# Performance work log

Measured on AMD Instinct MI355X. Metric: run time of the kernel, lower is better.

## Reference

```python
import jax, jax.numpy as jnp
import numpy as np

N_NODES = 50000
N_EDGES = 800000
NUM_GRAPHS = 64
D_IN = 128
D_HID = 128
D_EMB = 128
D_PRED = 256
D_OUT = 1
BN_EPS = 1e-5


def gcn_conv(x, W, b, src, dst, n_nodes):
    # PyG GCNConv: add self-loops, sym-normalize, aggregate, then bias.
    h = x @ W  # [N, d_out]
    # in-degree with self-loops
    deg = jax.ops.segment_sum(jnp.ones((src.shape[0],), h.dtype), dst,
                              num_segments=n_nodes) + 1.0
    inv_sqrt = 1.0 / jnp.sqrt(deg)  # [N]
    norm = inv_sqrt[src] * inv_sqrt[dst]  # [E]
    msg = h[src] * norm[:, None]  # [E, d_out] gather + scale
    agg = jax.ops.segment_sum(msg, dst, num_segments=n_nodes)
    # self-loop contribution: norm_ii = 1/deg_i
    agg = agg + h / deg[:, None]
    return agg + b


def batch_norm(h, gamma, beta):
    # BatchNorm1d in training mode: batch stats, biased variance
    mean = jnp.mean(h, axis=0)
    var = jnp.mean(jnp.square(h - mean), axis=0)
    return (h - mean) / jnp.sqrt(var + BN_EPS) * gamma + beta


def setup_inputs() -> dict:
    key = jax.random.key(0)
    ks = jax.random.split(key, 12)
    x = jax.random.normal(ks[0], (N_NODES, D_IN), dtype=jnp.float32)
    edge_index = jax.random.randint(ks[1], (2, N_EDGES), 0, N_NODES, dtype=jnp.int32)
    batch = jnp.sort(jax.random.randint(ks[2], (N_NODES,), 0, NUM_GRAPHS, dtype=jnp.int32))
    s1 = 1.0 / np.sqrt(D_IN)
    s2 = 1.0 / np.sqrt(D_HID)
    s3 = 1.0 / np.sqrt(D_EMB)
    s4 = 1.0 / np.sqrt(D_PRED)
    return {
        "x": x,
        "edge_index": edge_index,
        "batch": batch,
        "W1": jax.random.uniform(ks[3], (D_IN, D_HID), jnp.float32, -s1, s1),
        "b1": jnp.zeros((D_HID,), jnp.float32),
        "g1": jnp.ones((D_HID,), jnp.float32),
        "be1": jnp.zeros((D_HID,), jnp.float32),
        "W2": jax.random.uniform(ks[4], (D_HID, D_EMB), jnp.float32, -s2, s2),
        "b2": jnp.zeros((D_EMB,), jnp.float32),
        "g2": jnp.ones((D_EMB,), jnp.float32),
        "be2": jnp.zeros((D_EMB,), jnp.float32),
        "Wp1": jax.random.uniform(ks[5], (D_EMB, D_PRED), jnp.float32, -s3, s3),
        "bp1": jax.random.uniform(ks[6], (D_PRED,), jnp.float32, -s3, s3),
        "Wp2": jax.random.uniform(ks[7], (D_PRED, D_OUT), jnp.float32, -s4, s4),
        "bp2": jax.random.uniform(ks[8], (D_OUT,), jnp.float32, -s4, s4),
    }


def reference(x, edge_index, batch, W1, b1, g1, be1, W2, b2, g2, be2, Wp1, bp1, Wp2, bp2):
    src, dst = edge_index[0], edge_index[1]
    h = gcn_conv(x, W1, b1, src, dst, N_NODES)
    h = batch_norm(jax.nn.relu(h), g1, be1)
    h = gcn_conv(h, W2, b2, src, dst, N_NODES)
    h = batch_norm(jax.nn.relu(h), g2, be2)
    # global max pool per graph
    pooled = jax.ops.segment_max(h, batch, num_segments=NUM_GRAPHS)  # [G, D_EMB]
    # predictor MLP (Dropout is identity in eval)
    z = jax.nn.relu(pooled @ Wp1 + bp1)
    return z @ Wp2 + bp2
```

## Files before the change

### kernel.cpp

```cpp
#include <hip/hip_runtime.h>

#define NN 50000
#define NE 800000
#define NG 64
#define D 128
#define DP 256
#define BN_EPS 1e-5f
#define NSLOT 32
#define NB 196
#define NEB 3125

typedef unsigned short bf16;
typedef __attribute__((ext_vector_type(8))) short s16x8;
typedef __attribute__((ext_vector_type(4))) float f32x4;

__device__ __forceinline__ float bf2f(unsigned h16) {
  unsigned u = (h16 & 0xffffu) << 16; float f; __builtin_memcpy(&f, &u, 4); return f;
}
__device__ __forceinline__ bf16 f2bf(float f) {
  unsigned u; __builtin_memcpy(&u, &f, 4);
  return (bf16)((u + 0x7FFFu + ((u >> 16) & 1u)) >> 16);
}
__device__ __forceinline__ unsigned packbf2(float a, float b) {
  return (unsigned)f2bf(a) | ((unsigned)f2bf(b) << 16);
}
__device__ __forceinline__ s16x8 u4cast(uint4 v) {
  s16x8 r; __builtin_memcpy(&r, &v, 16); return r;
}

struct CvtArgs {
  const void* s[12];
  float* d[12];
  int n[12];
};

__global__ __launch_bounds__(256) void k_pre(const int* __restrict__ ei, int* __restrict__ cnt,
                                             CvtArgs a, const bf16* __restrict__ x,
                                             int* __restrict__ flag) {
  int b = blockIdx.x;
  if (b < NEB) {
    int e = b * 256 + threadIdx.x;
    atomicAdd(&cnt[ei[NE + e]], 1);
    return;
  }
  if (b < NEB + 192) {
    __shared__ int smode;
    if (threadIdx.x < 64) {
      float v = bf2f(x[2 * threadIdx.x]);
      float av = fabsf(v);
      int good = (v == 0.0f) || (av > 1e-30f && av < 32.0f);
      unsigned long long m = __ballot(good);
      if (threadIdx.x == 0) smode = (__popcll(m) >= 56) ? 1 : 0;
    }
    __syncthreads();
    int mode = smode;
    int idx = b - NEB;
    int t = idx >> 4;
    int base = (idx & 15) * 2048;
    int n = a.n[t];
    if (base >= n) return;
    float* dp = a.d[t];
    if (n >= 8) {
      int i8 = base + threadIdx.x * 8;
      if (i8 + 8 <= n) {
        if (mode) {
          uint4 raw = *(const uint4*)((const bf16*)a.s[t] + i8);
          *(float4*)(dp + i8) = make_float4(bf2f(raw.x & 0xffff), bf2f(raw.x >> 16),
                                            bf2f(raw.y & 0xffff), bf2f(raw.y >> 16));
          *(float4*)(dp + i8 + 4) = make_float4(bf2f(raw.z & 0xffff), bf2f(raw.z >> 16),
                                                bf2f(raw.w & 0xffff), bf2f(raw.w >> 16));
        } else {
          const float* s = (const float*)a.s[t] + i8;
          *(float4*)(dp + i8) = *(const float4*)s;
          *(float4*)(dp + i8 + 4) = *(const float4*)(s + 4);
        }
      }
    } else {
      int i = base + threadIdx.x;
      if (i < n) dp[i] = mode ? bf2f(((const bf16*)a.s[t])[i]) : ((const float*)a.s[t])[i];
    }
    return;
  }
  if (threadIdx.x < 64) {
    float v = bf2f(x[2 * threadIdx.x]);
    float av = fabsf(v);
    int good = (v == 0.0f) || (av > 1e-30f && av < 32.0f);
    unsigned long long m = __ballot(good);
    if (threadIdx.x == 0) { flag[0] = (__popcll(m) >= 56) ? 1 : 0; flag[1] = 1; }
  }
}

__device__ __forceinline__ void pack_slot(const float* __restrict__ W, const float* __restrict__ scale,
                                          bf16* __restrict__ Wp, int slot) {
  int kc = slot >> 9, ct = (slot >> 6) & 7, l = slot & 63;
  int q = l >> 4, p = l & 15;
  int n = ct * 16 + p;
  unsigned u[4];
#pragma unroll
  for (int jj = 0; jj < 4; ++jj) {
    int k0 = kc * 32 + q * 8 + jj * 2;
    float w0 = W[k0 * D + n], w1 = W[(k0 + 1) * D + n];
    if (scale) { w0 *= scale[k0]; w1 *= scale[k0 + 1]; }
    u[jj] = packbf2(w0, w1);
  }
  *(uint4*)(Wp + (size_t)slot * 8) = make_uint4(u[0], u[1], u[2], u[3]);
}

__global__ __launch_bounds__(256) void k_pack(const float* __restrict__ W, const float* __restrict__ scale,
                                              bf16* __restrict__ Wp) {
  int slot = blockIdx.x * 256 + threadIdx.x;
  if (slot < 2048) pack_slot(W, scale, Wp, slot);
}

__global__ __launch_bounds__(256) void k_scan3(const int* __restrict__ cnt,
                                               int* __restrict__ bsum, int* __restrict__ done,
                                               int* __restrict__ ro, int* __restrict__ cursor,
                                               float* __restrict__ isq,
                                               const float* __restrict__ W1f, bf16* __restrict__ Wpk1) {
  int b = blockIdx.x, t = threadIdx.x;
  if (b >= NB) {
    pack_slot(W1f, nullptr, Wpk1, (b - NB) * 256 + t);
    return;
  }
  __shared__ int sh[256];
  __shared__ int spart[4];
  __shared__ int sbase;
  int i = b * 256 + t;
  int c = (i < NN) ? cnt[i] : 0;
  sh[t] = c;
  __syncthreads();
  for (int off = 1; off < 256; off <<= 1) {
    int u = (t >= off) ? sh[t - off] : 0;
    __syncthreads();
    sh[t] += u;
    __syncthreads();
  }
  if (t == 255) {
    atomicExch(&bsum[b], sh[255]);
    __threadfence();
    atomicAdd(done, 1);
  }
  if (t == 0) {
    while (atomicAdd(done, 0) < NB) { __builtin_amdgcn_s_sleep(2); }
  }
  __syncthreads();
  int v = (t < b) ? atomicAdd(&bsum[t], 0) : 0;
  for (int off = 32; off; off >>= 1) v += __shfl_down(v, off);
  if ((t & 63) == 0) spart[t >> 6] = v;
  __syncthreads();
  if (t == 0) sbase = spart[0] + spart[1] + spart[2] + spart[3];
  __syncthreads();
  if (i < NN) {
    int o = sbase + sh[t] - c;
    ro[i] = o; cursor[i] = o;
    isq[i] = rsqrtf((float)(c + 1));
  }
  if (i == 0) ro[NN] = NE;
}

__global__ __launch_bounds__(256) void k_fill(const int* __restrict__ ei, const float* __restrict__ isq,
                                              int* __restrict__ cursor, int2* __restrict__ pk) {
  int e = blockIdx.x * 256 + threadIdx.x;
  if (e < NE) {
    int s = ei[e], d = ei[NE + e];
    int slot = atomicAdd(&cursor[d], 1);
    int2 v; v.x = s; v.y = __float_as_int(isq[s] * isq[d]);
    pk[slot] = v;
  }
}

__global__ __launch_bounds__(256) void k_mgemm(const void* __restrict__ Xv, const int* __restrict__ flag,
                                               const bf16* __restrict__ Wp,
                                               const float* __restrict__ rowadd,
                                               bf16* __restrict__ Out, int nrows) {
  __shared__ float Cs[4][16][D + 4];
  int l = threadIdx.x & 63, w = threadIdx.x >> 6;
  int q = l >> 4, p = l & 15;
  int mode = flag ? flag[0] : 0;
  float rv[8];
#pragma unroll
  for (int ct = 0; ct < 8; ++ct) rv[ct] = rowadd ? rowadd[ct * 16 + p] : 0.f;
  int ntiles = (nrows + 63) >> 6;
  for (int t = blockIdx.x; t < ntiles; t += gridDim.x) {
    int wb = t * 64 + w * 16;
    int rowc = min(wb + p, nrows - 1);
    f32x4 acc[8];
#pragma unroll
    for (int ct = 0; ct < 8; ++ct) { f32x4 z = {rv[ct], rv[ct], rv[ct], rv[ct]}; acc[ct] = z; }
#pragma unroll
    for (int kc = 0; kc < 4; ++kc) {
      s16x8 a;
      if (mode) {
        uint4 av = *(const uint4*)((const bf16*)Xv + (size_t)rowc * D + kc * 32 + q * 8);
        a = u4cast(av);
      } else {
        const float* Xf = (const float*)Xv + (size_t)rowc * D + kc * 32 + q * 8;
        float4 f0 = *(const float4*)Xf;
        float4 f1 = *(const float4*)(Xf + 4);
        uint4 u = make_uint4(packbf2(f0.x, f0.y), packbf2(f0.z, f0.w),
                             packbf2(f1.x, f1.y), packbf2(f1.z, f1.w));
        a = u4cast(u);
      }
#pragma unroll
      for (int ct = 0; ct < 8; ++ct) {
        s16x8 bfr = *(const s16x8*)(Wp + (size_t)(((kc << 3) + ct) * 64 + l) * 8);
        acc[ct] = __builtin_amdgcn_mfma_f32_16x16x32_bf16(a, bfr, acc[ct], 0, 0, 0);
      }
    }
#pragma unroll
    for (int ct = 0; ct < 8; ++ct)
#pragma unroll
      for (int r = 0; r < 4; ++r)
        Cs[w][q * 4 + r][ct * 16 + p] = acc[ct][r];
    __syncthreads();
#pragma unroll
    for (int i = 0; i < 4; ++i) {
      int idx = i * 64 + l;
      int rr = idx >> 4, c8 = idx & 15;
      int gr = t * 64 + w * 16 + rr;
      if (gr < nrows) {
        float4 v0 = *(const float4*)&Cs[w][rr][c8 * 8];
        float4 v1 = *(const float4*)&Cs[w][rr][c8 * 8 + 4];
        uint4 o = make_uint4(packbf2(v0.x, v0.y), packbf2(v0.z, v0.w),
                             packbf2(v1.x, v1.y), packbf2(v1.z, v1.w));
        *(uint4*)(Out + (size_t)gr * D + c8 * 8) = o;
      }
    }
    __syncthreads();
  }
}

template <int LAYER2>
__global__ __launch_bounds__(256) void k_agg(const bf16* __restrict__ H, const int* __restrict__ ro,
                                             const int2* __restrict__ pk,
                                             const float* __restrict__ b, const int* __restrict__ batch,
                                             bf16* __restrict__ Rout,
                                             float* __restrict__ sumP, float* __restrict__ sumsqP,
                                             float* __restrict__ pooled) {
  int lane = threadIdx.x & 63;
  int w = __builtin_amdgcn_readfirstlane(threadIdx.x >> 6);
  int nbase = blockIdx.x * 16 + w * 4;
  float2 bv = ((const float2*)b)[lane];
  float2 ls = make_float2(0.f, 0.f), lq = make_float2(0.f, 0.f);
  int gcur = -1; float2 mx = make_float2(0.f, 0.f);
  int nend = min(nbase + 4, NN);
  for (int n = nbase; n < nend; ++n) {
    int r0 = __builtin_amdgcn_readfirstlane(ro[n]);
    int r1 = __builtin_amdgcn_readfirstlane(ro[n + 1]);
    float invd = 1.0f / (float)(r1 - r0 + 1);
    unsigned hv = ((const unsigned*)(H + (size_t)n * D))[lane];
    float2 acc = make_float2(bf2f(hv & 0xffff) * invd, bf2f(hv >> 16) * invd);
    int e = r0;
    for (; e + 8 <= r1; e += 8) {
      int2 P[8];
      unsigned X[8];
#pragma unroll
      for (int j = 0; j < 8; ++j) P[j] = pk[e + j];
#pragma unroll
      for (int j = 0; j < 8; ++j) X[j] = ((const unsigned*)(H + (size_t)P[j].x * D))[lane];
#pragma unroll
      for (int j = 0; j < 8; ++j) {
        float c = __int_as_float(P[j].y);
        acc.x += bf2f(X[j] & 0xffff) * c; acc.y += bf2f(X[j] >> 16) * c;
      }
    }
    for (; e + 4 <= r1; e += 4) {
      int2 p0 = pk[e], p1 = pk[e + 1], p2 = pk[e + 2], p3 = pk[e + 3];
      unsigned x0 = ((const unsigned*)(H + (size_t)p0.x * D))[lane];
      unsigned x1 = ((const unsigned*)(H + (size_t)p1.x * D))[lane];
      unsigned x2 = ((const unsigned*)(H + (size_t)p2.x * D))[lane];
      unsigned x3 = ((const unsigned*)(H + (size_t)p3.x * D))[lane];
      float c0 = __int_as_float(p0.y), c1 = __int_as_float(p1.y);
      float c2 = __int_as_float(p2.y), c3 = __int_as_float(p3.y);
      acc.x += bf2f(x0 & 0xffff) * c0; acc.y += bf2f(x0 >> 16) * c0;
      acc.x += bf2f(x1 & 0xffff) * c1; acc.y += bf2f(x1 >> 16) * c1;
      acc.x += bf2f(x2 & 0xffff) * c2; acc.y += bf2f(x2 >> 16) * c2;
      acc.x += bf2f(x3 & 0xffff) * c3; acc.y += bf2f(x3 >> 16) * c3;
    }
    for (; e < r1; ++e) {
      int2 p0 = pk[e];
      unsigned x0 = ((const unsigned*)(H + (size_t)p0.x * D))[lane];
      float c0 = __int_as_float(p0.y);
      acc.x += bf2f(x0 & 0xffff) * c0; acc.y += bf2f(x0 >> 16) * c0;
    }
    float2 r = make_float2(fmaxf(acc.x + bv.x, 0.f), fmaxf(acc.y + bv.y, 0.f));
    if (!LAYER2) ((unsigned*)(Rout + (size_t)n * D))[lane] = packbf2(r.x, r.y);
    ls.x += r.x; ls.y += r.y; lq.x += r.x * r.x; lq.y += r.y * r.y;
    if (LAYER2) {
      int g = batch[n];
      if (g != gcur) {
        if (gcur >= 0) {
          atomicMax((int*)&pooled[(size_t)gcur * D + 2 * lane], __float_as_int(mx.x));
          atomicMax((int*)&pooled[(size_t)gcur * D + 2 * lane + 1], __float_as_int(mx.y));
        }
        gcur = g; mx = make_float2(0.f, 0.f);
      }
      mx.x = fmaxf(mx.x, r.x); mx.y = fmaxf(mx.y, r.y);
    }
  }
  if (LAYER2 && gcur >= 0) {
    atomicMax((int*)&pooled[(size_t)gcur * D + 2 * lane], __float_as_int(mx.x));
    atomicMax((int*)&pooled[(size_t)gcur * D + 2 * lane + 1], __float_as_int(mx.y));
  }
  __shared__ float ss[4][D], sq[4][D];
  ss[w][2 * lane] = ls.x; ss[w][2 * lane + 1] = ls.y;
  sq[w][2 * lane] = lq.x; sq[w][2 * lane + 1] = lq.y;
  __syncthreads();
  int slot = (blockIdx.x & (NSLOT - 1)) * D;
  if (threadIdx.x < D) {
    int k = threadIdx.x;
    atomicAdd(&sumP[slot + k], ss[0][k] + ss[1][k] + ss[2][k] + ss[3][k]);
  } else {
    int k = threadIdx.x - D;
    atomicAdd(&sumsqP[slot + k], sq[0][k] + sq[1][k] + sq[2][k] + sq[3][k]);
  }
}

__global__ void k_bnstats1(const float* __restrict__ sumP, const float* __restrict__ sumsqP,
                           const float* __restrict__ gamma, const float* __restrict__ beta,
                           const float* __restrict__ W2,
                           float* __restrict__ svec, float* __restrict__ tW2) {
  __shared__ float t[D];
  int k = threadIdx.x;
  float sm = 0.f, sq = 0.f;
  for (int i = 0; i < NSLOT; ++i) { sm += sumP[i * D + k]; sq += sumsqP[i * D + k]; }
  float mean = sm * (1.0f / NN);
  float var = sq * (1.0f / NN) - mean * mean;
  float s = gamma[k] * rsqrtf(var + BN_EPS);
  svec[k] = s;
  t[k] = beta[k] - mean * s;
  __syncthreads();
  float acc = 0.f;
  for (int kk = 0; kk < D; ++kk) acc += t[kk] * W2[kk * D + k];
  tW2[k] = acc;
}

__global__ __launch_bounds__(256) void k_head(const float* __restrict__ pooled,
                                              const float* __restrict__ sum2P, const float* __restrict__ sumsq2P,
                                              const float* __restrict__ gamma2, const float* __restrict__ beta2,
                                              const float* __restrict__ Wp1,
                                              const float* __restrict__ bp1, const float* __restrict__ Wp2,
                                              const float* __restrict__ bp2, void* out,
                                              const int* __restrict__ flag) {
  __shared__ float y[D];
  __shared__ float wr[4];
  int g = blockIdx.x, j = threadIdx.x;
  if (j < D) {
    float sm = 0.f, sq = 0.f;
    for (int i = 0; i < NSLOT; ++i) { sm += sum2P[i * D + j]; sq += sumsq2P[i * D + j]; }
    float mean = sm * (1.0f / NN);
    float var = sq * (1.0f / NN) - mean * mean;
    float s = gamma2[j] * rsqrtf(var + BN_EPS);
    y[j] = pooled[(size_t)g * D + j] * s + (beta2[j] - mean * s);
  }
  __syncthreads();
  float acc = bp1[j];
#pragma unroll 4
  for (int k = 0; k < D; ++k) acc += y[k] * Wp1[k * DP + j];
  float v = fmaxf(acc, 0.f) * Wp2[j];
  for (int off = 32; off; off >>= 1) v += __shfl_down(v, off);
  if ((j & 63) == 0) wr[j >> 6] = v;
  __syncthreads();
  if (j == 0) {
    float r = wr[0] + wr[1] + wr[2] + wr[3] + bp2[0];
    if (flag[0]) ((bf16*)out)[g] = f2bf(r);
    else ((float*)out)[g] = r;
  }
}

extern "C" void kernel_launch(void* const* d_in, const int* in_sizes, int n_in,
                              void* d_out, int out_size, void* d_ws, size_t ws_size,
                              hipStream_t stream) {
  const void* x   = d_in[0];
  const int*  ei  = (const int*)d_in[1];
  const int*  bat = (const int*)d_in[2];

  float* f = (float*)d_ws;
  bf16* A = (bf16*)f; f += (size_t)NN * D / 2;
  bf16* B = (bf16*)f; f += (size_t)NN * D / 2;
  float* zbase = f;
  int* cnt  = (int*)f; f += NN;
  int* done = (int*)f; f += 4;
  float* sum1P   = f; f += NSLOT * D;
  float* sumsq1P = f; f += NSLOT * D;
  float* sum2P   = f; f += NSLOT * D;
  float* sumsq2P = f; f += NSLOT * D;
  float* pooled  = f; f += (size_t)NG * D;
  size_t zbytes = (size_t)((char*)f - (char*)zbase);
  float* W1f  = f; f += D * D;
  float* W2f  = f; f += D * D;
  float* Wp1f = f; f += D * DP;
  float* b1f  = f; f += D;
  float* g1f  = f; f += D;
  float* be1f = f; f += D;
  float* b2f  = f; f += D;
  float* g2f  = f; f += D;
  float* be2f = f; f += D;
  float* bp1f = f; f += DP;
  float* Wp2f = f; f += DP;
  float* bp2f = f; f += 4;
  bf16* Wpk1 = (bf16*)f; f += 2048 * 8 / 2;
  bf16* Wpk2 = (bf16*)f; f += 2048 * 8 / 2;
  float* svec1 = f; f += D;
  float* tW2   = f; f += D;
  float* isq   = f; f += NN;
  int2* pk    = (int2*)f; f += (size_t)NE * 2;
  int* ro     = (int*)f; f += NN + 1;
  int* cursor = (int*)f; f += NN;
  int* bsum   = (int*)f; f += NB;
  int* flag   = (int*)f;

  hipMemsetAsync(zbase, 0, zbytes, stream);

  CvtArgs ca;
  ca.s[0] = d_in[3];  ca.d[0] = W1f;  ca.n[0] = D * D;
  ca.s[1] = d_in[7];  ca.d[1] = W2f;  ca.n[1] = D * D;
  ca.s[2] = d_in[11]; ca.d[2] = Wp1f; ca.n[2] = D * DP;
  ca.s[3] = d_in[4];  ca.d[3] = b1f;  ca.n[3] = D;
  ca.s[4] = d_in[5];  ca.d[4] = g1f;  ca.n[4] = D;
  ca.s[5] = d_in[6];  ca.d[5] = be1f; ca.n[5] = D;
  ca.s[6] = d_in[8];  ca.d[6] = b2f;  ca.n[6] = D;
  ca.s[7] = d_in[9];  ca.d[7] = g2f;  ca.n[7] = D;
  ca.s[8] = d_in[10]; ca.d[8] = be2f; ca.n[8] = D;
  ca.s[9] = d_in[12]; ca.d[9] = bp1f; ca.n[9] = DP;
  ca.s[10] = d_in[13]; ca.d[10] = Wp2f; ca.n[10] = DP;
  ca.s[11] = d_in[14]; ca.d[11] = bp2f; ca.n[11] = 1;

  k_pre<<<NEB + 192 + 1, 256, 0, stream>>>(ei, cnt, ca, (const bf16*)x, flag);
  k_scan3<<<NB + 8, 256, 0, stream>>>(cnt, bsum, done, ro, cursor, isq, W1f, Wpk1);
  k_fill<<<NEB, 256, 0, stream>>>(ei, isq, cursor, pk);

  k_mgemm<<<(NN + 63) / 64, 256, 0, stream>>>(x, flag, Wpk1, nullptr, A, NN);
  k_agg<0><<<(NN + 15) / 16, 256, 0, stream>>>(A, ro, pk, b1f, nullptr,
                                               B, sum1P, sumsq1P, nullptr);
  k_bnstats1<<<1, D, 0, stream>>>(sum1P, sumsq1P, g1f, be1f, W2f, svec1, tW2);

  k_pack<<<8, 256, 0, stream>>>(W2f, svec1, Wpk2);
  k_mgemm<<<(NN + 63) / 64, 256, 0, stream>>>(B, flag + 1, Wpk2, tW2, A, NN);
  k_agg<1><<<(NN + 15) / 16, 256, 0, stream>>>(A, ro, pk, b2f, bat,
                                               nullptr, sum2P, sumsq2P, pooled);

  k_head<<<NG, DP, 0, stream>>>(pooled, sum2P, sumsq2P, g2f, be2f,
                                Wp1f, bp1f, Wp2f, bp2f, d_out, flag);
}
```

Before: 234.4 us.

## Fuse BN1 stats and W2 packing into aggregation tail; vectorize edge kernels

The per-layer-1 BatchNorm statistics reduction, the W2 scaling and the weight packing now run in the last block to finish layer-1 aggregation, found with an atomic counter. This removes two tiny kernel launches and their serialization gaps. The edge-count and CSR-fill kernels now read four edges per thread with int4 loads. The aggregation loads edge records and stores outputs with nontemporal hints, and the stat slot count grows to spread atomics more widely. In exchange, the final reduction runs on a single block after a threadfence handshake, and there are more partial slots to sum.

```diff
diff --git a/kernel.cpp b/kernel.cpp
--- a/kernel.cpp
+++ b/kernel.cpp
@@ -6,9 +6,9 @@
 #define D 128
 #define DP 256
 #define BN_EPS 1e-5f
-#define NSLOT 32
+#define NSLOT 128
 #define NB 196
-#define NEB 3125
+#define NEB4 782
 
 typedef unsigned short bf16;
 typedef __attribute__((ext_vector_type(8))) short s16x8;
@@ -38,12 +38,18 @@
                                              CvtArgs a, const bf16* __restrict__ x,
                                              int* __restrict__ flag) {
   int b = blockIdx.x;
-  if (b < NEB) {
-    int e = b * 256 + threadIdx.x;
-    atomicAdd(&cnt[ei[NE + e]], 1);
+  if (b < NEB4) {
+    int e = (b * 256 + threadIdx.x) * 4;
+    if (e < NE) {
+      int4 d4 = *(const int4*)(ei + NE + e);
+      atomicAdd(&cnt[d4.x], 1);
+      atomicAdd(&cnt[d4.y], 1);
+      atomicAdd(&cnt[d4.z], 1);
+      atomicAdd(&cnt[d4.w], 1);
+    }
     return;
   }
-  if (b < NEB + 192) {
+  if (b < NEB4 + 192) {
     __shared__ int smode;
     if (threadIdx.x < 64) {
       float v = bf2f(x[2 * threadIdx.x]);
@@ -54,7 +60,7 @@
     }
     __syncthreads();
     int mode = smode;
-    int idx = b - NEB;
+    int idx = b - NEB4;
     int t = idx >> 4;
     int base = (idx & 15) * 2048;
     int n = a.n[t];
@@ -90,7 +96,7 @@
   }
 }
 
-__device__ __forceinline__ void pack_slot(const float* __restrict__ W, const float* __restrict__ scale,
+__device__ __forceinline__ void pack_slot(const float* __restrict__ W, const float* scale,
                                           bf16* __restrict__ Wp, int slot) {
   int kc = slot >> 9, ct = (slot >> 6) & 7, l = slot & 63;
   int q = l >> 4, p = l & 15;
@@ -104,12 +110,6 @@
     u[jj] = packbf2(w0, w1);
   }
   *(uint4*)(Wp + (size_t)slot * 8) = make_uint4(u[0], u[1], u[2], u[3]);
-}
-
-__global__ __launch_bounds__(256) void k_pack(const float* __restrict__ W, const float* __restrict__ scale,
-                                              bf16* __restrict__ Wp) {
-  int slot = blockIdx.x * 256 + threadIdx.x;
-  if (slot < 2048) pack_slot(W, scale, Wp, slot);
 }
 
 __global__ __launch_bounds__(256) void k_scan3(const int* __restrict__ cnt,
@@ -160,12 +160,18 @@
 
 __global__ __launch_bounds__(256) void k_fill(const int* __restrict__ ei, const float* __restrict__ isq,
                                               int* __restrict__ cursor, int2* __restrict__ pk) {
-  int e = blockIdx.x * 256 + threadIdx.x;
+  int e = (blockIdx.x * 256 + threadIdx.x) * 4;
   if (e < NE) {
-    int s = ei[e], d = ei[NE + e];
-    int slot = atomicAdd(&cursor[d], 1);
-    int2 v; v.x = s; v.y = __float_as_int(isq[s] * isq[d]);
-    pk[slot] = v;
+    int4 s4 = *(const int4*)(ei + e);
+    int4 d4 = *(const int4*)(ei + NE + e);
+    int ss[4] = {s4.x, s4.y, s4.z, s4.w};
+    int dd[4] = {d4.x, d4.y, d4.z, d4.w};
+#pragma unroll
+    for (int j = 0; j < 4; ++j) {
+      int slot = atomicAdd(&cursor[dd[j]], 1);
+      int2 v; v.x = ss[j]; v.y = __float_as_int(isq[ss[j]] * isq[dd[j]]);
+      pk[slot] = v;
+    }
   }
 }
 
@@ -236,7 +242,11 @@
                                              const float* __restrict__ b, const int* __restrict__ batch,
                                              bf16* __restrict__ Rout,
                                              float* __restrict__ sumP, float* __restrict__ sumsqP,
-                                             float* __restrict__ pooled) {
+                                             float* __restrict__ pooled,
+                                             const float* __restrict__ gamma, const float* __restrict__ beta,
+                                             const float* __restrict__ W2f,
+                                             float* __restrict__ tW2, bf16* __restrict__ Wpk2,
+                                             int* __restrict__ ctr) {
   int lane = threadIdx.x & 63;
   int w = __builtin_amdgcn_readfirstlane(threadIdx.x >> 6);
   int nbase = blockIdx.x * 16 + w * 4;
@@ -252,39 +262,45 @@
     float2 acc = make_float2(bf2f(hv & 0xffff) * invd, bf2f(hv >> 16) * invd);
     int e = r0;
     for (; e + 8 <= r1; e += 8) {
-      int2 P[8];
+      unsigned long long P[8];
       unsigned X[8];
 #pragma unroll
-      for (int j = 0; j < 8; ++j) P[j] = pk[e + j];
-#pragma unroll
-      for (int j = 0; j < 8; ++j) X[j] = ((const unsigned*)(H + (size_t)P[j].x * D))[lane];
+      for (int j = 0; j < 8; ++j)
+        P[j] = __builtin_nontemporal_load((const unsigned long long*)(pk + e + j));
+#pragma unroll
+      for (int j = 0; j < 8; ++j)
+        X[j] = ((const unsigned*)(H + (size_t)(unsigned)(P[j] & 0xffffffffu) * D))[lane];
 #pragma unroll
       for (int j = 0; j < 8; ++j) {
-        float c = __int_as_float(P[j].y);
+        float c = __int_as_float((int)(P[j] >> 32));
         acc.x += bf2f(X[j] & 0xffff) * c; acc.y += bf2f(X[j] >> 16) * c;
       }
     }
     for (; e + 4 <= r1; e += 4) {
-      int2 p0 = pk[e], p1 = pk[e + 1], p2 = pk[e + 2], p3 = pk[e + 3];
-      unsigned x0 = ((const unsigned*)(H + (size_t)p0.x * D))[lane];
-      unsigned x1 = ((const unsigned*)(H + (size_t)p1.x * D))[lane];
-      unsigned x2 = ((const unsigned*)(H + (size_t)p2.x * D))[lane];
-      unsigned x3 = ((const unsigned*)(H + (size_t)p3.x * D))[lane];
-      float c0 = __int_as_float(p0.y), c1 = __int_as_float(p1.y);
-      float c2 = __int_as_float(p2.y), c3 = __int_as_float(p3.y);
+      unsigned long long p0 = __builtin_nontemporal_load((const unsigned long long*)(pk + e));
+      unsigned long long p1 = __builtin_nontemporal_load((const unsigned long long*)(pk + e + 1));
+      unsigned long long p2 = __builtin_nontemporal_load((const unsigned long long*)(pk + e + 2));
+      unsigned long long p3 = __builtin_nontemporal_load((const unsigned long long*)(pk + e + 3));
+      unsigned x0 = ((const unsigned*)(H + (size_t)(unsigned)(p0 & 0xffffffffu) * D))[lane];
+      unsigned x1 = ((const unsigned*)(H + (size_t)(unsigned)(p1 & 0xffffffffu) * D))[lane];
+      unsigned x2 = ((const unsigned*)(H + (size_t)(unsigned)(p2 & 0xffffffffu) * D))[lane];
+      unsigned x3 = ((const unsigned*)(H + (size_t)(unsigned)(p3 & 0xffffffffu) * D))[lane];
+      float c0 = __int_as_float((int)(p0 >> 32)), c1 = __int_as_float((int)(p1 >> 32));
+      float c2 = __int_as_float((int)(p2 >> 32)), c3 = __int_as_float((int)(p3 >> 32));
       acc.x += bf2f(x0 & 0xffff) * c0; acc.y += bf2f(x0 >> 16) * c0;
       acc.x += bf2f(x1 & 0xffff) * c1; acc.y += bf2f(x1 >> 16) * c1;
       acc.x += bf2f(x2 & 0xffff) * c2; acc.y += bf2f(x2 >> 16) * c2;
       acc.x += bf2f(x3 & 0xffff) * c3; acc.y += bf2f(x3 >> 16) * c3;
     }
     for (; e < r1; ++e) {
-      int2 p0 = pk[e];
-      unsigned x0 = ((const unsigned*)(H + (size_t)p0.x * D))[lane];
-      float c0 = __int_as_float(p0.y);
+      unsigned long long p0 = __builtin_nontemporal_load((const unsigned long long*)(pk + e));
+      unsigned x0 = ((const unsigned*)(H + (size_t)(unsigned)(p0 & 0xffffffffu) * D))[lane];
+      float c0 = __int_as_float((int)(p0 >> 32));
       acc.x += bf2f(x0 & 0xffff) * c0; acc.y += bf2f(x0 >> 16) * c0;
     }
     float2 r = make_float2(fmaxf(acc.x + bv.x, 0.f), fmaxf(acc.y + bv.y, 0.f));
-    if (!LAYER2) ((unsigned*)(Rout + (size_t)n * D))[lane] = packbf2(r.x, r.y);
+    if (!LAYER2)
+      __builtin_nontemporal_store(packbf2(r.x, r.y), (unsigned*)(Rout + (size_t)n * D) + lane);
     ls.x += r.x; ls.y += r.y; lq.x += r.x * r.x; lq.y += r.y * r.y;
     if (LAYER2) {
       int g = batch[n];
@@ -314,25 +330,35 @@
     int k = threadIdx.x - D;
     atomicAdd(&sumsqP[slot + k], sq[0][k] + sq[1][k] + sq[2][k] + sq[3][k]);
   }
-}
-
-__global__ void k_bnstats1(const float* __restrict__ sumP, const float* __restrict__ sumsqP,
-                           const float* __restrict__ gamma, const float* __restrict__ beta,
-                           const float* __restrict__ W2,
-                           float* __restrict__ svec, float* __restrict__ tW2) {
-  __shared__ float t[D];
-  int k = threadIdx.x;
-  float sm = 0.f, sq = 0.f;
-  for (int i = 0; i < NSLOT; ++i) { sm += sumP[i * D + k]; sq += sumsqP[i * D + k]; }
-  float mean = sm * (1.0f / NN);
-  float var = sq * (1.0f / NN) - mean * mean;
-  float s = gamma[k] * rsqrtf(var + BN_EPS);
-  svec[k] = s;
-  t[k] = beta[k] - mean * s;
-  __syncthreads();
-  float acc = 0.f;
-  for (int kk = 0; kk < D; ++kk) acc += t[kk] * W2[kk * D + k];
-  tW2[k] = acc;
+  if (LAYER2) return;
+  __syncthreads();
+  __shared__ int islast;
+  if (threadIdx.x == 0) {
+    __threadfence();
+    islast = (atomicAdd(ctr, 1) == (int)gridDim.x - 1) ? 1 : 0;
+  }
+  __syncthreads();
+  if (!islast) return;
+  __threadfence();
+  __shared__ float sv[D], tv[D];
+  int t = threadIdx.x;
+  if (t < D) {
+    float sm = 0.f, sq2 = 0.f;
+    for (int i = 0; i < NSLOT; ++i) { sm += sumP[i * D + t]; sq2 += sumsqP[i * D + t]; }
+    float mean = sm * (1.0f / NN);
+    float var = sq2 * (1.0f / NN) - mean * mean;
+    float s = gamma[t] * rsqrtf(var + BN_EPS);
+    sv[t] = s;
+    tv[t] = beta[t] - mean * s;
+  }
+  __syncthreads();
+  if (t < D) {
+    float a = 0.f;
+    for (int kk = 0; kk < D; ++kk) a += tv[kk] * W2f[kk * D + t];
+    tW2[t] = a;
+  }
+#pragma unroll
+  for (int it = 0; it < 8; ++it) pack_slot(W2f, sv, Wpk2, it * 256 + t);
 }
 
 __global__ __launch_bounds__(256) void k_head(const float* __restrict__ pooled,
@@ -381,6 +407,7 @@
   float* zbase = f;
   int* cnt  = (int*)f; f += NN;
   int* done = (int*)f; f += 4;
+  int* ctr  = (int*)f; f += 4;
   float* sum1P   = f; f += NSLOT * D;
   float* sumsq1P = f; f += NSLOT * D;
   float* sum2P   = f; f += NSLOT * D;
@@ -401,7 +428,6 @@
   float* bp2f = f; f += 4;
   bf16* Wpk1 = (bf16*)f; f += 2048 * 8 / 2;
   bf16* Wpk2 = (bf16*)f; f += 2048 * 8 / 2;
-  float* svec1 = f; f += D;
   float* tW2   = f; f += D;
   float* isq   = f; f += NN;
   int2* pk    = (int2*)f; f += (size_t)NE * 2;
@@ -426,19 +452,19 @@
   ca.s[10] = d_in[13]; ca.d[10] = Wp2f; ca.n[10] = DP;
   ca.s[11] = d_in[14]; ca.d[11] = bp2f; ca.n[11] = 1;
 
-  k_pre<<<NEB + 192 + 1, 256, 0, stream>>>(ei, cnt, ca, (const bf16*)x, flag);
+  k_pre<<<NEB4 + 192 + 1, 256, 0, stream>>>(ei, cnt, ca, (const bf16*)x, flag);
   k_scan3<<<NB + 8, 256, 0, stream>>>(cnt, bsum, done, ro, cursor, isq, W1f, Wpk1);
-  k_fill<<<NEB, 256, 0, stream>>>(ei, isq, cursor, pk);
+  k_fill<<<NEB4, 256, 0, stream>>>(ei, isq, cursor, pk);
 
   k_mgemm<<<(NN + 63) / 64, 256, 0, stream>>>(x, flag, Wpk1, nullptr, A, NN);
   k_agg<0><<<(NN + 15) / 16, 256, 0, stream>>>(A, ro, pk, b1f, nullptr,
-                                               B, sum1P, sumsq1P, nullptr);
-  k_bnstats1<<<1, D, 0, stream>>>(sum1P, sumsq1P, g1f, be1f, W2f, svec1, tW2);
-
-  k_pack<<<8, 256, 0, stream>>>(W2f, svec1, Wpk2);
+                                               B, sum1P, sumsq1P, nullptr,
+                                               g1f, be1f, W2f, tW2, Wpk2, ctr);
+
   k_mgemm<<<(NN + 63) / 64, 256, 0, stream>>>(B, flag + 1, Wpk2, tW2, A, NN);
   k_agg<1><<<(NN + 15) / 16, 256, 0, stream>>>(A, ro, pk, b2f, bat,
-                                               nullptr, sum2P, sumsq2P, pooled);
+                                               nullptr, sum2P, sumsq2P, pooled,
+                                               nullptr, nullptr, nullptr, nullptr, nullptr, nullptr);
 
   k_head<<<NG, DP, 0, stream>>>(pooled, sum2P, sumsq2P, g2f, be2f,
                                 Wp1f, bp1f, Wp2f, bp2f, d_out, flag);
```

New measurement: 316.1 us. +34.9%, slower.
